# Optimization experiments

Measured on AMD Instinct MI355X. Metric: run time of the kernel, lower is better.

Reference implementation:

```python
import jax, jax.numpy as jnp
import numpy as np

FF = 2          # freqfold
HALF_FF = 1     # ff // 2

def _fold_k(t, G, ff):
    # t: [N, G, D] -> real/imag each [N, nband, G*ff]
    N, _, D = t.shape
    Df = D // 2
    nband = Df // ff
    t = jnp.swapaxes(t, -1, -2)  # [N, D, G]
    def fold(x):  # x: [N, Df, G]
        x = x.reshape(N, nband, ff, G).transpose(0, 2, 1, 3)  # [N, ff, nband, G]
        return x.reshape(N, nband, G * ff)
    return fold(t[:, :Df, :]), fold(t[:, Df:, :])

def _fold_q(t, G, groups, ff):
    # t: [N, H, D] with H = G*groups -> real/imag each [N, groups, nband, G*ff]
    N, H, D = t.shape
    Df = D // 2
    nband = Df // ff
    t = t.reshape(N, G, groups, D).transpose(0, 2, 1, 3)  # [N, groups, G, D]
    t = jnp.swapaxes(t, -1, -2)                            # [N, groups, D, G]
    def fold(x):  # x: [N, groups, Df, G]
        x = x.reshape(N, groups, nband, ff, G).transpose(0, 1, 3, 2, 4)  # [N, groups, ff, nband, G]
        return x.reshape(N, groups, nband, G * ff)
    return fold(t[:, :, :Df, :]), fold(t[:, :, Df:, :])

def setup_inputs() -> dict:
    key = jax.random.key(0)
    ks = jax.random.split(key, 8)
    N, H, G, D, r = 8192, 32, 8, 128, 4
    ff = FF
    nband = D // (2 * ff)
    gff = G * ff
    nope_in = G * D - D // 2
    return {
        "q": jax.random.normal(ks[0], (N, H, D), jnp.float32),
        "k": jax.random.normal(ks[1], (N, G, D), jnp.float32),
        "v": jax.random.normal(ks[2], (N, G, D), jnp.float32),
        "q_orig": jax.random.normal(ks[3], (N, H, D), jnp.float32),
        "k_orig": jax.random.normal(ks[4], (N, G, D), jnp.float32),
        "qk_index_proj": 0.02 * jax.random.normal(ks[5], (nband, gff, gff), jnp.float32),
        "qk_nope_proj_w": 0.02 * jax.random.normal(ks[6], (D // 2, nope_in), jnp.float32),
        "v_transform": 0.02 * jax.random.normal(ks[7], (H, D, r), jnp.float32),
    }

def reference(q, k, v, q_orig, k_orig, qk_index_proj, qk_nope_proj_w, v_transform):
    N, H, D = q.shape
    G = k.shape[1]
    groups = H // G
    ff, half_ff = FF, HALF_FF
    nband = D // (2 * ff)
    nope_cols = G * ff - half_ff
    qk_w = qk_index_proj

    # ---- rope path (post-RoPE q, k) ----
    kr_re, kr_im = _fold_k(k, G, ff)
    kr_re_p = jnp.einsum('bnf,nfr->bnr', kr_re, qk_w)
    kr_im_p = jnp.einsum('bnf,nfr->bnr', kr_im, qk_w)
    index_k_rope = jnp.concatenate([
        kr_re_p[:, :, :half_ff].reshape(N, nband * half_ff),
        kr_im_p[:, :, :half_ff].reshape(N, nband * half_ff)], axis=-1)

    qr_re, qr_im = _fold_q(q, G, groups, ff)
    qr_re_p = jnp.einsum('tgnf,nfr->tgnr', qr_re, qk_w)
    qr_im_p = jnp.einsum('tgnf,nfr->tgnr', qr_im, qk_w)
    index_q_rope = jnp.concatenate([
        qr_re_p[:, :, :, :half_ff].reshape(N, groups, nband * half_ff),
        qr_im_p[:, :, :, :half_ff].reshape(N, groups, nband * half_ff)], axis=-1)

    # ---- nope path (pre-RoPE q_orig, k_orig) ----
    kn_re, kn_im = _fold_k(k_orig, G, ff)
    kn_re_p = jnp.einsum('bnf,nfr->bnr', kn_re, qk_w)
    kn_im_p = jnp.einsum('bnf,nfr->bnr', kn_im, qk_w)
    k_nope_rotary = jnp.concatenate([
        kn_re_p[:, :, half_ff:].reshape(N, nband * nope_cols),
        kn_im_p[:, :, half_ff:].reshape(N, nband * nope_cols)], axis=-1)
    k_nope_lr = k_nope_rotary @ qk_nope_proj_w.T
    index_k = jnp.concatenate([index_k_rope, k_nope_lr], axis=-1)  # [N, D]

    qn_re, qn_im = _fold_q(q_orig, G, groups, ff)
    qn_re_p = jnp.einsum('tgnf,nfr->tgnr', qn_re, qk_w)
    qn_im_p = jnp.einsum('tgnf,nfr->tgnr', qn_im, qk_w)
    q_nope_rotary = jnp.concatenate([
        qn_re_p[:, :, :, half_ff:].reshape(N, groups, nband * nope_cols),
        qn_im_p[:, :, :, half_ff:].reshape(N, groups, nband * nope_cols)], axis=-1)
    q_nope_lr = q_nope_rotary @ qk_nope_proj_w.T
    index_q = jnp.concatenate([index_q_rope, q_nope_lr], axis=-1)  # [N, groups, D]

    # ---- per-head weights from V ----
    r = v_transform.shape[-1]
    v_h = jnp.repeat(v, groups, axis=1)  # [N, H, D]
    w = jnp.einsum('nhd,hdr->nhr', v_h, v_transform)
    w = w.reshape(N, G, groups, r).transpose(0, 2, 1, 3).reshape(N, groups, G * r)
    weights = jnp.linalg.norm(w.astype(jnp.float32), axis=-1)  # [N, groups]

    return index_q, index_k, weights
```

## Files before the change

kernel.cpp:

```cpp
#include <hip/hip_runtime.h>
#include <math.h>

namespace {
constexpr int N_TOK  = 8192;
constexpr int GROUPS = 4;
constexpr int D      = 128;
}

typedef short v8s __attribute__((ext_vector_type(8)));
typedef float v4f __attribute__((ext_vector_type(4)));

__device__ __forceinline__ short f2bf(float f) {
    union { float f; unsigned u; } x; x.f = f;
    unsigned r = x.u + 0x7FFFu + ((x.u >> 16) & 1u);
    return (short)(r >> 16);
}

__global__ __launch_bounds__(256)
void build_MT(const float* __restrict__ widx,
              const float* __restrict__ wn,
              short* __restrict__ MT)
{
    const int idx = blockIdx.x * 256 + threadIdx.x;
    const int col = idx >> 10;
    const int kk  = idx & 1023;
    const int g   = kk >> 7;
    const int dp  = kk & 127;
    const int part = dp >> 6;
    const int dpp  = dp & 63;
    const int B    = (dpp & 1) * 16 + (dpp >> 2);
    const int c    = g + 8 * ((dpp >> 1) & 1);

    float val;
    if (col < 64) {
        val = (col == part * 32 + B) ? widx[B * 256 + c * 16] : 0.f;
    } else {
        const int d2 = col - 64;
        const float* wrow = wn + d2 * 960 + part * 480 + B * 15;
        const float* wi   = widx + B * 256 + c * 16;
        float s = 0.f;
#pragma unroll
        for (int o = 1; o < 16; ++o) s += wi[o] * wrow[o - 1];
        val = s;
    }
    MT[idx] = f2bf(val);
}

__global__ __launch_bounds__(256, 4)
void gemm_kernel(const float* __restrict__ q,
                 const float* __restrict__ k,
                 const float* __restrict__ q_orig,
                 const float* __restrict__ k_orig,
                 const short* __restrict__ MT,
                 float* __restrict__ out_iq,
                 float* __restrict__ out_ik)
{
    const int lane = threadIdx.x & 63;
    const int wave = threadIdx.x >> 6;
    const int m    = lane & 15;
    const int quad = lane >> 4;
    const int half = blockIdx.x & 1;
    const int base_row = (blockIdx.x >> 1) * 64 + wave * 16;

    const int row = base_row + m;
    const int n   = row / 5;
    const int jj  = row - n * 5;
    const bool isq = (jj < 4);
    const float* ap;
    if (half == 0) ap = isq ? (q      + n * 4096 + jj * 128) : (k      + n * 1024);
    else           ap = isq ? (q_orig + n * 4096 + jj * 128) : (k_orig + n * 1024);

    const short* bbase = MT + (half * 64 + m) * 1024;

    v4f acc[4];
#pragma unroll
    for (int t = 0; t < 4; ++t) acc[t] = (v4f){0.f, 0.f, 0.f, 0.f};

#pragma unroll 4
    for (int ks = 0; ks < 32; ++ks) {
        const int kk   = ks * 32 + quad * 8;
        const int offA = isq ? ((kk >> 7) * 512 + (kk & 127)) : kk;
        const float4 r0 = *(const float4*)(ap + offA);
        const float4 r1 = *(const float4*)(ap + offA + 4);
        v8s a;
        a[0] = f2bf(r0.x); a[1] = f2bf(r0.y); a[2] = f2bf(r0.z); a[3] = f2bf(r0.w);
        a[4] = f2bf(r1.x); a[5] = f2bf(r1.y); a[6] = f2bf(r1.z); a[7] = f2bf(r1.w);

        const short* bp = bbase + kk;
#pragma unroll
        for (int t = 0; t < 4; ++t) {
            const v8s b = *(const v8s*)(bp + t * 16384);
            acc[t] = __builtin_amdgcn_mfma_f32_16x16x32_bf16(a, b, acc[t], 0, 0, 0);
        }
    }

#pragma unroll
    for (int t = 0; t < 4; ++t) {
        const int col = half * 64 + t * 16 + m;
#pragma unroll
        for (int i = 0; i < 4; ++i) {
            const int r2  = base_row + quad * 4 + i;
            const int n2  = r2 / 5;
            const int jj2 = r2 - n2 * 5;
            float* dst = (jj2 < 4) ? (out_iq + n2 * 512 + jj2 * 128)
                                   : (out_ik + n2 * 128);
            dst[col] = acc[t][i];
        }
    }
}

__global__ __launch_bounds__(512)
void weights_kernel(const float* __restrict__ v,
                    const float* __restrict__ vt,
                    float* __restrict__ out_w)
{
    __shared__ float4 s_vt[4096];
    const int tid = threadIdx.x;

    const float4* vt4 = (const float4*)vt;
#pragma unroll
    for (int i0 = 0; i0 < 8; ++i0) {
        const int i   = i0 * 512 + tid;
        const int hh  = i >> 7;
        const int low = i & 127;
        s_vt[(i & ~127) | (low ^ (hh & 7))] = vt4[i];
    }
    __syncthreads();

    const int tok_l = tid & 15;
    const int h     = tid >> 4;
    const int g     = h >> 2;
    const int sw    = h & 7;
    const int token = blockIdx.x * 16 + tok_l;

    const float4* vrow = (const float4*)(v + token * 1024 + g * 128);
    const float4* wrow = s_vt + h * 128;

    float ax = 0.f, ay = 0.f, az = 0.f, aw = 0.f;
#pragma unroll 8
    for (int d4 = 0; d4 < 32; ++d4) {
        const float4 vv = vrow[d4];
        {
            const float4 w0 = wrow[(d4 * 4 + 0) ^ sw];
            ax += vv.x * w0.x; ay += vv.x * w0.y; az += vv.x * w0.z; aw += vv.x * w0.w;
        }
        {
            const float4 w1 = wrow[(d4 * 4 + 1) ^ sw];
            ax += vv.y * w1.x; ay += vv.y * w1.y; az += vv.y * w1.z; aw += vv.y * w1.w;
        }
        {
            const float4 w2 = wrow[(d4 * 4 + 2) ^ sw];
            ax += vv.z * w2.x; ay += vv.z * w2.y; az += vv.z * w2.z; aw += vv.z * w2.w;
        }
        {
            const float4 w3 = wrow[(d4 * 4 + 3) ^ sw];
            ax += vv.w * w3.x; ay += vv.w * w3.y; az += vv.w * w3.z; aw += vv.w * w3.w;
        }
    }
    const float s = ax * ax + ay * ay + az * az + aw * aw;

    __syncthreads();
    float* s_red = (float*)s_vt;
    s_red[tok_l * 32 + h] = s;
    __syncthreads();
    if (tid < 64) {
        const int tok = tid & 15;
        const int j   = tid >> 4;
        const float* p = s_red + tok * 32 + j;
        float t = 0.f;
#pragma unroll
        for (int g2 = 0; g2 < 8; ++g2) t += p[g2 * 4];
        out_w[(blockIdx.x * 16 + tok) * 4 + j] = sqrtf(t);
    }
}

extern "C" void kernel_launch(void* const* d_in, const int* in_sizes, int n_in,
                              void* d_out, int out_size, void* d_ws, size_t ws_size,
                              hipStream_t stream) {
    const float* q      = (const float*)d_in[0];
    const float* k      = (const float*)d_in[1];
    const float* v      = (const float*)d_in[2];
    const float* q_orig = (const float*)d_in[3];
    const float* k_orig = (const float*)d_in[4];
    const float* widx   = (const float*)d_in[5];
    const float* wn     = (const float*)d_in[6];
    const float* vt     = (const float*)d_in[7];

    float* out_iq = (float*)d_out;
    float* out_ik = out_iq + (size_t)N_TOK * GROUPS * D;
    float* out_w  = out_ik + (size_t)N_TOK * D;

    short* MT = (short*)d_ws;

    hipLaunchKernelGGL(build_MT, dim3(512), dim3(256), 0, stream, widx, wn, MT);
    hipLaunchKernelGGL(gemm_kernel, dim3(1280), dim3(256), 0, stream,
                       q, k, q_orig, k_orig, MT, out_iq, out_ik);
    hipLaunchKernelGGL(weights_kernel, dim3(512), dim3(512), 0, stream,
                       v, vt, out_w);
}
```

Baseline: 390.2 us.

## Stage A tiles via global_load_lds double buffering with XOR-swizzled LDS

Replaces direct per-lane float4 global loads of the A operand with async global-to-LDS copies (global_load_lds), double-buffered over 16 K-chunks of 64 floats, with an XOR swizzle to avoid bank conflicts. This is meant to coalesce the row-strided q/k reads and overlap the next chunk's fetch with MFMA work. It also raises the occupancy hint from 4 to 5 blocks per CU. The cost is 32 KB of LDS per block, which may limit how many blocks fit per CU, plus a block-wide barrier every chunk.

New measurement: 448.4 us. 14.9% more time.

```diff
diff --git a/kernel.cpp b/kernel.cpp
--- a/kernel.cpp
+++ b/kernel.cpp
@@ -9,6 +9,9 @@
 
 typedef short v8s __attribute__((ext_vector_type(8)));
 typedef float v4f __attribute__((ext_vector_type(4)));
+
+typedef const __attribute__((address_space(1))) unsigned g_u32;
+typedef __attribute__((address_space(3))) unsigned l_u32;
 
 __device__ __forceinline__ short f2bf(float f) {
     union { float f; unsigned u; } x; x.f = f;
@@ -46,7 +49,7 @@
     MT[idx] = f2bf(val);
 }
 
-__global__ __launch_bounds__(256, 4)
+__global__ __launch_bounds__(256, 5)
 void gemm_kernel(const float* __restrict__ q,
                  const float* __restrict__ k,
                  const float* __restrict__ q_orig,
@@ -55,6 +58,8 @@
                  float* __restrict__ out_iq,
                  float* __restrict__ out_ik)
 {
+    __shared__ float lds[2][4096];
+
     const int lane = threadIdx.x & 63;
     const int wave = threadIdx.x >> 6;
     const int m    = lane & 15;
@@ -62,13 +67,20 @@
     const int half = blockIdx.x & 1;
     const int base_row = (blockIdx.x >> 1) * 64 + wave * 16;
 
-    const int row = base_row + m;
-    const int n   = row / 5;
-    const int jj  = row - n * 5;
-    const bool isq = (jj < 4);
-    const float* ap;
-    if (half == 0) ap = isq ? (q      + n * 4096 + jj * 128) : (k      + n * 1024);
-    else           ap = isq ? (q_orig + n * 4096 + jj * 128) : (k_orig + n * 1024);
+    const float* qsrc = half ? q_orig : q;
+    const float* ksrc = half ? k_orig : k;
+
+    const float* gp[4];
+    int isq_[4];
+#pragma unroll
+    for (int j = 0; j < 4; ++j) {
+        const int r  = base_row + j * 4 + (lane >> 4);
+        const int n  = r / 5;
+        const int jj = r - n * 5;
+        const int sx = (lane & 15) ^ (r & 15);
+        if (jj < 4) { isq_[j] = 1; gp[j] = qsrc + n * 4096 + jj * 128 + sx * 4; }
+        else        { isq_[j] = 0; gp[j] = ksrc + n * 1024 + sx * 4; }
+    }
 
     const short* bbase = MT + (half * 64 + m) * 1024;
 
@@ -76,22 +88,45 @@
 #pragma unroll
     for (int t = 0; t < 4; ++t) acc[t] = (v4f){0.f, 0.f, 0.f, 0.f};
 
-#pragma unroll 4
-    for (int ks = 0; ks < 32; ++ks) {
-        const int kk   = ks * 32 + quad * 8;
-        const int offA = isq ? ((kk >> 7) * 512 + (kk & 127)) : kk;
-        const float4 r0 = *(const float4*)(ap + offA);
-        const float4 r1 = *(const float4*)(ap + offA + 4);
-        v8s a;
-        a[0] = f2bf(r0.x); a[1] = f2bf(r0.y); a[2] = f2bf(r0.z); a[3] = f2bf(r0.w);
-        a[4] = f2bf(r1.x); a[5] = f2bf(r1.y); a[6] = f2bf(r1.z); a[7] = f2bf(r1.w);
-
-        const short* bp = bbase + kk;
-#pragma unroll
-        for (int t = 0; t < 4; ++t) {
-            const v8s b = *(const v8s*)(bp + t * 16384);
-            acc[t] = __builtin_amdgcn_mfma_f32_16x16x32_bf16(a, b, acc[t], 0, 0, 0);
-        }
+    auto stage = [&](int c, int buf) {
+        const int qoff = (c >> 1) * 512 + (c & 1) * 64;
+        const int koff = c * 64;
+#pragma unroll
+        for (int j = 0; j < 4; ++j) {
+            const float* g = gp[j] + (isq_[j] ? qoff : koff);
+            __builtin_amdgcn_global_load_lds(
+                (g_u32*)g,
+                (l_u32*)&lds[buf][(wave * 4 + j) * 256],
+                16, 0, 0);
+        }
+    };
+
+    stage(0, 0);
+    __syncthreads();
+
+#pragma unroll 2
+    for (int c = 0; c < 16; ++c) {
+        const int buf = c & 1;
+        if (c < 15) stage(c + 1, buf ^ 1);
+
+        const float* Ab = &lds[buf][(wave * 16 + m) * 64];
+#pragma unroll
+        for (int ks2 = 0; ks2 < 2; ++ks2) {
+            const int s0 = ks2 * 8 + quad * 2;
+            const float4 a0 = *(const float4*)(Ab + (((s0    ) ^ m) << 2));
+            const float4 a1 = *(const float4*)(Ab + (((s0 + 1) ^ m) << 2));
+            v8s a;
+            a[0] = f2bf(a0.x); a[1] = f2bf(a0.y); a[2] = f2bf(a0.z); a[3] = f2bf(a0.w);
+            a[4] = f2bf(a1.x); a[5] = f2bf(a1.y); a[6] = f2bf(a1.z); a[7] = f2bf(a1.w);
+
+            const short* bp = bbase + c * 64 + ks2 * 32 + quad * 8;
+#pragma unroll
+            for (int t = 0; t < 4; ++t) {
+                const v8s b = *(const v8s*)(bp + t * 16384);
+                acc[t] = __builtin_amdgcn_mfma_f32_16x16x32_bf16(a, b, acc[t], 0, 0, 0);
+            }
+        }
+        __syncthreads();
     }
 
 #pragma unroll
```
